# Performance work log

Measured on AMD Instinct MI355X. Metric: run time of the kernel, lower is better.

The kernel has to match this reference:

```python
import jax, jax.numpy as jnp
import numpy as np

B, S, D = 4, 4096, 1024
H, EXPAND, DCONV = 8, 2, 4
DI = D * EXPAND           # d_inner = 2048
HD = DI // H              # head_dim = 256
LN_EPS = 1e-5


def setup_inputs() -> dict:
    key = jax.random.key(0)
    ks = jax.random.split(key, 6)
    scale = lambda fan_in: 1.0 / np.sqrt(fan_in)
    return {
        "x": jax.random.normal(ks[0], (B, S, D), dtype=jnp.float32),
        "norm_w": jnp.ones((D,), dtype=jnp.float32),
        "norm_b": jnp.zeros((D,), dtype=jnp.float32),
        "in_proj_w": jax.random.normal(ks[1], (2 * DI, D), dtype=jnp.float32) * scale(D),
        "conv_w": jax.random.normal(ks[2], (DI, 1, DCONV), dtype=jnp.float32) * scale(DCONV),
        "conv_b": jax.random.normal(ks[3], (DI,), dtype=jnp.float32) * 0.02,
        "out_proj_w": jax.random.normal(ks[4], (D, DI), dtype=jnp.float32) * scale(DI),
        "log_alpha": jax.random.uniform(ks[5], (H,), dtype=jnp.float32,
                                        minval=np.log(0.1), maxval=np.log(0.99)),
    }


def reference(x, norm_w, norm_b, in_proj_w, conv_w, conv_b, out_proj_w, log_alpha):
    residual = x
    # LayerNorm
    mu = jnp.mean(x, axis=-1, keepdims=True)
    var = jnp.var(x, axis=-1, keepdims=True)
    xn = (x - mu) * jax.lax.rsqrt(var + LN_EPS) * norm_w + norm_b
    # input projection -> [B, S, 2*DI]
    xz = jnp.einsum("bsd,ed->bse", xn, in_proj_w)
    x_path, gate = xz[..., :DI], xz[..., DI:]
    # causal depthwise conv1d (torch pads d_conv-1 both sides then slices [:S])
    kernel = jnp.transpose(conv_w, (2, 1, 0))  # [DCONV, 1, DI] (WIO)
    x_path = jax.lax.conv_general_dilated(
        x_path, kernel, window_strides=(1,), padding=[(DCONV - 1, 0)],
        dimension_numbers=("NWC", "WIO", "NWC"), feature_group_count=DI,
    ) + conv_b
    # multi-head scalar-decay linear recurrence: y_t = alpha*y_{t-1} + x_t
    xh = x_path.reshape(B, S, H, HD)
    alpha = jax.nn.sigmoid(log_alpha)[:, None]  # [H, 1]

    def step(y, xt):
        y = alpha * y + xt
        return y, y

    y0 = jnp.zeros((B, H, HD), dtype=x.dtype)
    _, ys = jax.lax.scan(step, y0, jnp.transpose(xh, (1, 0, 2, 3)))  # [S, B, H, HD]
    x_path = jnp.transpose(ys, (1, 0, 2, 3)).reshape(B, S, DI)
    # gate + output projection (dropout in eval mode = identity)
    x_path = jax.nn.silu(x_path) * gate
    out = jnp.einsum("bse,de->bsd", x_path, out_proj_w)
    return out + residual
```

## Files before the change

### kernel.cpp

```cpp
#include <hip/hip_runtime.h>
#include <hip/hip_bf16.h>
#include <cstdint>

#define Bb 4
#define Ss 4096
#define Dd 1024
#define Hh 8
#define DI 2048
#define HD 256
#define XZN 4096
#define Mtot 16384
#define NCH 128
#define CHUNK 32

typedef __bf16 bf16_t;
typedef __bf16 bf16x8 __attribute__((ext_vector_type(8)));
typedef __bf16 bf16x4 __attribute__((ext_vector_type(4)));
typedef float f32x4 __attribute__((ext_vector_type(4)));

__device__ __forceinline__ float sigmoidf_(float x) { return 1.f / (1.f + __expf(-x)); }

__device__ __forceinline__ void async_ld16(void* lds, const void* g) {
  __builtin_amdgcn_global_load_lds(
      (const __attribute__((address_space(1))) void*)(uintptr_t)g,
      (__attribute__((address_space(3))) void*)(uint32_t)(uintptr_t)lds,
      16, 0, 0);
}

__global__ __launch_bounds__(256) void cvt_kernel(const float* __restrict__ s,
                                                  bf16_t* __restrict__ d) {
  const int i = blockIdx.x * 256 + threadIdx.x;
  const float4 v = ((const float4*)s)[i];
  bf16_t* o = d + 4 * (size_t)i;
  o[0] = (bf16_t)v.x; o[1] = (bf16_t)v.y; o[2] = (bf16_t)v.z; o[3] = (bf16_t)v.w;
}

__global__ __launch_bounds__(256) void ln_kernel(const float* __restrict__ x,
                                                 const float* __restrict__ w,
                                                 const float* __restrict__ b,
                                                 bf16_t* __restrict__ xn) {
  __shared__ float red[8];
  const int row = blockIdx.x;
  const float4 v = ((const float4*)(x + (size_t)row * Dd))[threadIdx.x];
  float s  = v.x + v.y + v.z + v.w;
  float s2 = v.x * v.x + v.y * v.y + v.z * v.z + v.w * v.w;
  #pragma unroll
  for (int off = 32; off; off >>= 1) { s += __shfl_down(s, off); s2 += __shfl_down(s2, off); }
  const int wave = threadIdx.x >> 6, lane = threadIdx.x & 63;
  if (lane == 0) { red[wave * 2] = s; red[wave * 2 + 1] = s2; }
  __syncthreads();
  if (threadIdx.x == 0) {
    float S = 0.f, S2 = 0.f;
    for (int i = 0; i < 4; ++i) { S += red[i * 2]; S2 += red[i * 2 + 1]; }
    red[0] = S; red[1] = S2;
  }
  __syncthreads();
  const float mean = red[0] * (1.f / Dd);
  const float var  = red[1] * (1.f / Dd) - mean * mean;
  const float rstd = rsqrtf(var + 1e-5f);
  const float4 wv = ((const float4*)w)[threadIdx.x];
  const float4 bv = ((const float4*)b)[threadIdx.x];
  bf16_t* o = xn + (size_t)row * Dd + threadIdx.x * 4;
  o[0] = (bf16_t)((v.x - mean) * rstd * wv.x + bv.x);
  o[1] = (bf16_t)((v.y - mean) * rstd * wv.y + bv.y);
  o[2] = (bf16_t)((v.z - mean) * rstd * wv.z + bv.z);
  o[3] = (bf16_t)((v.w - mean) * rstd * wv.w + bv.w);
}

template <int ADD_RES>
__global__ __launch_bounds__(512, 2) void gemm256(const bf16_t* __restrict__ A,
                                                  const bf16_t* __restrict__ Bw,
                                                  void* __restrict__ Cv,
                                                  const float* __restrict__ res,
                                                  int M, int N, int K) {
  __shared__ __align__(16) bf16_t As[4][8192];
  __shared__ __align__(16) bf16_t Bs[4][8192];
  const int tid = threadIdx.x;
  const int wave = tid >> 6, lane = tid & 63;
  const int wm = wave >> 2, wn = wave & 3;

  const int nbx = gridDim.x;
  const int nwg = nbx * gridDim.y;
  const int bid0 = blockIdx.y * nbx + blockIdx.x;
  const int cpx = nwg >> 3;
  const int bid = (bid0 & 7) * cpx + (bid0 >> 3);
  const int bm = bid / nbx, bn = bid % nbx;

  f32x4 acc[8][4];
  #pragma unroll
  for (int i = 0; i < 8; ++i)
    #pragma unroll
    for (int j = 0; j < 4; ++j) acc[i][j] = (f32x4){0.f, 0.f, 0.f, 0.f};

  const int srow = tid >> 2;
  const int sc   = (tid & 3) ^ ((tid >> 3) & 3);
  const bf16_t* Ag = A  + (size_t)(bm * 256 + srow) * K + sc * 8;
  const bf16_t* Bg = Bw + (size_t)(bn * 256 + srow) * K + sc * 8;
  const size_t rowK128 = (size_t)128 * K;
  char* const AsB = (char*)As + (wave << 10);
  char* const BsB = (char*)Bs + (wave << 10);

  const int fr = lane & 15, fq = lane >> 4;
  int aoff[8], boff[4];
  #pragma unroll
  for (int mt = 0; mt < 8; ++mt) {
    const int row = wm * 128 + mt * 16 + fr;
    aoff[mt] = row * 64 + ((fq ^ ((row >> 1) & 3)) << 4);
  }
  #pragma unroll
  for (int nt = 0; nt < 4; ++nt) {
    const int row = wn * 64 + nt * 16 + fr;
    boff[nt] = row * 64 + ((fq ^ ((row >> 1) & 3)) << 4);
  }

  const int NT = K >> 5;
  #pragma unroll
  for (int t = 0; t < 3; ++t) {
    const int kt = t << 5;
    async_ld16(AsB + t * 16384,        Ag + kt);
    async_ld16(AsB + t * 16384 + 8192, Ag + rowK128 + kt);
    async_ld16(BsB + t * 16384,        Bg + kt);
    async_ld16(BsB + t * 16384 + 8192, Bg + rowK128 + kt);
  }

  for (int t = 0; t < NT; ++t) {
    const int rem = NT - 1 - t;
    if (rem >= 2)      asm volatile("s_waitcnt vmcnt(8)" ::: "memory");
    else if (rem == 1) asm volatile("s_waitcnt vmcnt(4)" ::: "memory");
    else               asm volatile("s_waitcnt vmcnt(0)" ::: "memory");
    __builtin_amdgcn_s_barrier();

    const int buf = t & 3;
    const char* Ab = (const char*)As + buf * 16384;
    const char* Bbp = (const char*)Bs + buf * 16384;
    bf16x8 af[8], bfv[4];
    #pragma unroll
    for (int mt = 0; mt < 8; ++mt) af[mt] = *(const bf16x8*)(Ab + aoff[mt]);
    #pragma unroll
    for (int nt = 0; nt < 4; ++nt) bfv[nt] = *(const bf16x8*)(Bbp + boff[nt]);

    if (t + 3 < NT) {
      const int b = (t + 3) & 3;
      const int kt = (t + 3) << 5;
      async_ld16(AsB + b * 16384,        Ag + kt);
      async_ld16(AsB + b * 16384 + 8192, Ag + rowK128 + kt);
      async_ld16(BsB + b * 16384,        Bg + kt);
      async_ld16(BsB + b * 16384 + 8192, Bg + rowK128 + kt);
    }

    __builtin_amdgcn_s_setprio(1);
    #pragma unroll
    for (int mt = 0; mt < 8; ++mt)
      #pragma unroll
      for (int nt = 0; nt < 4; ++nt)
        acc[mt][nt] =
            __builtin_amdgcn_mfma_f32_16x16x32_bf16(af[mt], bfv[nt], acc[mt][nt], 0, 0, 0);
    __builtin_amdgcn_s_setprio(0);
  }

  const int m0 = bm * 256 + wm * 128 + fq * 4;
  const int n0 = bn * 256 + wn * 64 + fr;
  #pragma unroll
  for (int mt = 0; mt < 8; ++mt)
    #pragma unroll
    for (int nt = 0; nt < 4; ++nt)
      #pragma unroll
      for (int r = 0; r < 4; ++r) {
        const size_t m = (size_t)(m0 + mt * 16 + r);
        const size_t n = (size_t)(n0 + nt * 16);
        if (ADD_RES)
          ((float*)Cv)[m * N + n] = acc[mt][nt][r] + res[m * N + n];
        else
          ((bf16_t*)Cv)[m * N + n] = (bf16_t)acc[mt][nt][r];
      }
}

__global__ __launch_bounds__(256) void scanA_kernel(const bf16_t* __restrict__ xz,
                                                    const float* __restrict__ conv_w,
                                                    const float* __restrict__ conv_b,
                                                    const float* __restrict__ log_alpha,
                                                    float* __restrict__ carry) {
  const int half  = blockIdx.x & 1;
  const int chunk = (blockIdx.x >> 1) & (NCH - 1);
  const int b     = blockIdx.x >> 8;
  const int ch    = half * 1024 + threadIdx.x * 4;
  const float alpha = sigmoidf_(log_alpha[ch >> 8]);
  float w[4][4], bias[4];
  #pragma unroll
  for (int j = 0; j < 4; ++j) {
    const float4 cw = ((const float4*)conv_w)[ch + j];
    w[j][0] = cw.x; w[j][1] = cw.y; w[j][2] = cw.z; w[j][3] = cw.w;
    bias[j] = conv_b[ch + j];
  }
  const int s0 = chunk * CHUNK;
  const size_t base = ((size_t)b * Ss + s0) * XZN + ch;
  float x3[4] = {0,0,0,0}, x2[4] = {0,0,0,0}, x1[4] = {0,0,0,0}, y[4] = {0,0,0,0};
  if (chunk > 0) {
    const bf16x4 v3 = *(const bf16x4*)(xz + base - 3 * (size_t)XZN);
    const bf16x4 v2 = *(const bf16x4*)(xz + base - 2 * (size_t)XZN);
    const bf16x4 v1 = *(const bf16x4*)(xz + base - 1 * (size_t)XZN);
    #pragma unroll
    for (int j = 0; j < 4; ++j) { x3[j] = (float)v3[j]; x2[j] = (float)v2[j]; x1[j] = (float)v1[j]; }
  }
  #pragma unroll 4
  for (int t = 0; t < CHUNK; ++t) {
    const bf16x4 v = *(const bf16x4*)(xz + base + (size_t)t * XZN);
    #pragma unroll
    for (int j = 0; j < 4; ++j) {
      const float xc = (float)v[j];
      const float cv = bias[j] + w[j][0] * x3[j] + w[j][1] * x2[j] + w[j][2] * x1[j] + w[j][3] * xc;
      x3[j] = x2[j]; x2[j] = x1[j]; x1[j] = xc;
      y[j] = fmaf(alpha, y[j], cv);
    }
  }
  *(float4*)(carry + ((size_t)b * NCH + chunk) * DI + ch) =
      make_float4(y[0], y[1], y[2], y[3]);
}

__global__ __launch_bounds__(256) void scanB_kernel(const float* __restrict__ carry,
                                                    float* __restrict__ carryin,
                                                    const float* __restrict__ log_alpha) {
  __shared__ float S[8][32];
  const int b   = blockIdx.x >> 6;
  const int chg = blockIdx.x & 63;
  const int cg  = threadIdx.x >> 5;
  const int chl = threadIdx.x & 31;
  const int ch  = chg * 32 + chl;
  const float alpha = sigmoidf_(log_alpha[ch >> 8]);
  const float lal  = log2f(alpha);
  const float aL   = exp2f((float)CHUNK * lal);
  const float aL16 = exp2f((float)(CHUNK * 16) * lal);
  const size_t base = ((size_t)b * NCH + cg * 16) * DI + ch;
  float v[16];
  #pragma unroll
  for (int i = 0; i < 16; ++i) v[i] = carry[base + (size_t)i * DI];
  float Sl = v[0];
  #pragma unroll
  for (int i = 1; i < 16; ++i) Sl = fmaf(aL, Sl, v[i]);
  S[cg][chl] = Sl;
  __syncthreads();
  float P = 0.f;
  for (int h = 0; h < cg; ++h) P = fmaf(aL16, P, S[h][chl]);
  #pragma unroll
  for (int i = 0; i < 16; ++i) {
    carryin[base + (size_t)i * DI] = P;
    P = fmaf(aL, P, v[i]);
  }
}

__global__ __launch_bounds__(256) void scanC_kernel(const bf16_t* __restrict__ xz,
                                                    const float* __restrict__ conv_w,
                                                    const float* __restrict__ conv_b,
                                                    const float* __restrict__ log_alpha,
                                                    const float* __restrict__ carryin,
                                                    bf16_t* __restrict__ act) {
  const int half  = blockIdx.x & 1;
  const int chunk = (blockIdx.x >> 1) & (NCH - 1);
  const int b     = blockIdx.x >> 8;
  const int ch    = half * 1024 + threadIdx.x * 4;
  const float alpha = sigmoidf_(log_alpha[ch >> 8]);
  float w[4][4], bias[4];
  #pragma unroll
  for (int j = 0; j < 4; ++j) {
    const float4 cw = ((const float4*)conv_w)[ch + j];
    w[j][0] = cw.x; w[j][1] = cw.y; w[j][2] = cw.z; w[j][3] = cw.w;
    bias[j] = conv_b[ch + j];
  }
  const int s0 = chunk * CHUNK;
  const size_t base = ((size_t)b * Ss + s0) * XZN + ch;
  float x3[4] = {0,0,0,0}, x2[4] = {0,0,0,0}, x1[4] = {0,0,0,0}, y[4];
  const float4 cin = *(const float4*)(carryin + ((size_t)b * NCH + chunk) * DI + ch);
  y[0] = cin.x; y[1] = cin.y; y[2] = cin.z; y[3] = cin.w;
  if (chunk > 0) {
    const bf16x4 v3 = *(const bf16x4*)(xz + base - 3 * (size_t)XZN);
    const bf16x4 v2 = *(const bf16x4*)(xz + base - 2 * (size_t)XZN);
    const bf16x4 v1 = *(const bf16x4*)(xz + base - 1 * (size_t)XZN);
    #pragma unroll
    for (int j = 0; j < 4; ++j) { x3[j] = (float)v3[j]; x2[j] = (float)v2[j]; x1[j] = (float)v1[j]; }
  }
  const size_t abase = ((size_t)b * Ss + s0) * DI + ch;
  #pragma unroll 4
  for (int t = 0; t < CHUNK; ++t) {
    const bf16x4 v = *(const bf16x4*)(xz + base + (size_t)t * XZN);
    const bf16x4 gv = *(const bf16x4*)(xz + base + (size_t)t * XZN + DI);
    bf16x4 ov;
    #pragma unroll
    for (int j = 0; j < 4; ++j) {
      const float xc = (float)v[j];
      const float cv = bias[j] + w[j][0] * x3[j] + w[j][1] * x2[j] + w[j][2] * x1[j] + w[j][3] * xc;
      x3[j] = x2[j]; x2[j] = x1[j]; x1[j] = xc;
      y[j] = fmaf(alpha, y[j], cv);
      const float o = y[j] * (1.f / (1.f + __expf(-y[j]))) * (float)gv[j];
      ov[j] = (bf16_t)o;
    }
    *(bf16x4*)(act + abase + (size_t)t * DI) = ov;
  }
}

extern "C" void kernel_launch(void* const* d_in, const int* in_sizes, int n_in,
                              void* d_out, int out_size, void* d_ws, size_t ws_size,
                              hipStream_t stream) {
  const float* x          = (const float*)d_in[0];
  const float* norm_w     = (const float*)d_in[1];
  const float* norm_b     = (const float*)d_in[2];
  const float* in_proj_w  = (const float*)d_in[3];
  const float* conv_w     = (const float*)d_in[4];
  const float* conv_b     = (const float*)d_in[5];
  const float* out_proj_w = (const float*)d_in[6];
  const float* log_alpha  = (const float*)d_in[7];
  float* out = (float*)d_out;

  char* ws = (char*)d_ws;
  bf16_t* xn     = (bf16_t*)(ws);
  bf16_t* w_in   = (bf16_t*)(ws + 33554432);
  bf16_t* w_out  = (bf16_t*)(ws + 41943040);
  bf16_t* xz     = (bf16_t*)(ws + 46137344);
  bf16_t* act    = (bf16_t*)(ws + 180355072);
  float*  carry   = (float*)(ws);
  float*  carryin = (float*)(ws + 4194304);

  cvt_kernel<<<4096, 256, 0, stream>>>(in_proj_w, w_in);
  cvt_kernel<<<2048, 256, 0, stream>>>(out_proj_w, w_out);
  ln_kernel<<<Mtot, 256, 0, stream>>>(x, norm_w, norm_b, xn);

  dim3 g1(XZN / 256, Mtot / 256);
  gemm256<0><<<g1, 512, 0, stream>>>(xn, w_in, xz, nullptr, Mtot, XZN, Dd);

  scanA_kernel<<<Bb * NCH * 2, 256, 0, stream>>>(xz, conv_w, conv_b, log_alpha, carry);
  scanB_kernel<<<Bb * 64, 256, 0, stream>>>(carry, carryin, log_alpha);
  scanC_kernel<<<Bb * NCH * 2, 256, 0, stream>>>(xz, conv_w, conv_b, log_alpha, carryin, act);

  dim3 g2(Dd / 256, Mtot / 256);
  gemm256<1><<<g2, 512, 0, stream>>>(act, w_out, out, x, Mtot, Dd, DI);
}
```

Before: 407.8 us.

## Restructure GEMM main loop into double-buffered BK=64 ping-pong with interleaved staging

Replaces the 4-stage BK=32 ring of LDS buffers with two 64-wide K buffers. Each K-half's A fragments are split into two groups of four, and async global->LDS stores for the next tile are issued between fragment reads and MFMA groups. This lowers register pressure by holding fewer A fragments at once and spreads memory issue across the compute. In exchange the prefetch depth drops to one tile ahead and explicit lgkmcnt waits are added, which may expose more global latency; LDS use stays at 128KB per block.

```diff
diff --git a/kernel.cpp b/kernel.cpp
--- a/kernel.cpp
+++ b/kernel.cpp
@@ -73,8 +73,7 @@
                                                   void* __restrict__ Cv,
                                                   const float* __restrict__ res,
                                                   int M, int N, int K) {
-  __shared__ __align__(16) bf16_t As[4][8192];
-  __shared__ __align__(16) bf16_t Bs[4][8192];
+  __shared__ __align__(16) char LDS[131072];
   const int tid = threadIdx.x;
   const int wave = tid >> 6, lane = tid & 63;
   const int wm = wave >> 2, wn = wave & 3;
@@ -92,13 +91,11 @@
     #pragma unroll
     for (int j = 0; j < 4; ++j) acc[i][j] = (f32x4){0.f, 0.f, 0.f, 0.f};
 
-  const int srow = tid >> 2;
-  const int sc   = (tid & 3) ^ ((tid >> 3) & 3);
-  const bf16_t* Ag = A  + (size_t)(bm * 256 + srow) * K + sc * 8;
-  const bf16_t* Bg = Bw + (size_t)(bn * 256 + srow) * K + sc * 8;
+  const int scg = (lane & 3) ^ ((lane >> 3) & 3);
+  const bf16_t* Ag = A  + (size_t)(bm * 256 + wave * 16 + (lane >> 2)) * K + scg * 8;
+  const bf16_t* Bg = Bw + (size_t)(bn * 256 + wave * 16 + (lane >> 2)) * K + scg * 8;
   const size_t rowK128 = (size_t)128 * K;
-  char* const AsB = (char*)As + (wave << 10);
-  char* const BsB = (char*)Bs + (wave << 10);
+  char* const LDSw = LDS + wave * 1024;
 
   const int fr = lane & 15, fq = lane >> 4;
   int aoff[8], boff[4];
@@ -113,50 +110,87 @@
     boff[nt] = row * 64 + ((fq ^ ((row >> 1) & 3)) << 4);
   }
 
-  const int NT = K >> 5;
-  #pragma unroll
-  for (int t = 0; t < 3; ++t) {
-    const int kt = t << 5;
-    async_ld16(AsB + t * 16384,        Ag + kt);
-    async_ld16(AsB + t * 16384 + 8192, Ag + rowK128 + kt);
-    async_ld16(BsB + t * 16384,        Bg + kt);
-    async_ld16(BsB + t * 16384 + 8192, Bg + rowK128 + kt);
-  }
-
-  for (int t = 0; t < NT; ++t) {
-    const int rem = NT - 1 - t;
-    if (rem >= 2)      asm volatile("s_waitcnt vmcnt(8)" ::: "memory");
-    else if (rem == 1) asm volatile("s_waitcnt vmcnt(4)" ::: "memory");
-    else               asm volatile("s_waitcnt vmcnt(0)" ::: "memory");
-    __builtin_amdgcn_s_barrier();
-
-    const int buf = t & 3;
-    const char* Ab = (const char*)As + buf * 16384;
-    const char* Bbp = (const char*)Bs + buf * 16384;
-    bf16x8 af[8], bfv[4];
-    #pragma unroll
-    for (int mt = 0; mt < 8; ++mt) af[mt] = *(const bf16x8*)(Ab + aoff[mt]);
-    #pragma unroll
-    for (int nt = 0; nt < 4; ++nt) bfv[nt] = *(const bf16x8*)(Bbp + boff[nt]);
-
-    if (t + 3 < NT) {
-      const int b = (t + 3) & 3;
-      const int kt = (t + 3) << 5;
-      async_ld16(AsB + b * 16384,        Ag + kt);
-      async_ld16(AsB + b * 16384 + 8192, Ag + rowK128 + kt);
-      async_ld16(BsB + b * 16384,        Bg + kt);
-      async_ld16(BsB + b * 16384 + 8192, Bg + rowK128 + kt);
-    }
-
-    __builtin_amdgcn_s_setprio(1);
-    #pragma unroll
-    for (int mt = 0; mt < 8; ++mt)
-      #pragma unroll
-      for (int nt = 0; nt < 4; ++nt)
-        acc[mt][nt] =
-            __builtin_amdgcn_mfma_f32_16x16x32_bf16(af[mt], bfv[nt], acc[mt][nt], 0, 0, 0);
-    __builtin_amdgcn_s_setprio(0);
-  }
+  const int NT = K >> 6;
+
+#define STG(u, mat, ks) do {                                              \
+    char* d_ = LDSw + ((u) & 1) * 65536 + (mat) * 32768 + (ks) * 16384;   \
+    const bf16_t* s_ = (mat) ? Bg : Ag;                                   \
+    const int ko_ = (u) * 64 + (ks) * 32;                                 \
+    async_ld16(d_,        s_ + ko_);                                      \
+    async_ld16(d_ + 8192, s_ + rowK128 + ko_);                            \
+  } while (0)
+
+#define RDA(DST, bufb, ks, g) do {                                        \
+    _Pragma("unroll")                                                     \
+    for (int i_ = 0; i_ < 4; ++i_)                                        \
+      DST[i_] = *(const bf16x8*)(LDS + (bufb) * 65536 + (ks) * 16384 + aoff[(g) * 4 + i_]); \
+  } while (0)
+
+#define RDB(DST, bufb, ks) do {                                           \
+    _Pragma("unroll")                                                     \
+    for (int i_ = 0; i_ < 4; ++i_)                                        \
+      DST[i_] = *(const bf16x8*)(LDS + (bufb) * 65536 + 32768 + (ks) * 16384 + boff[i_]); \
+  } while (0)
+
+#define MM(AF, BF, g) do {                                                \
+    __builtin_amdgcn_s_setprio(1);                                        \
+    _Pragma("unroll")                                                     \
+    for (int m_ = 0; m_ < 4; ++m_)                                        \
+      _Pragma("unroll")                                                   \
+      for (int n_ = 0; n_ < 4; ++n_)                                      \
+        acc[(g) * 4 + m_][n_] = __builtin_amdgcn_mfma_f32_16x16x32_bf16(  \
+            AF[m_], BF[n_], acc[(g) * 4 + m_][n_], 0, 0, 0);              \
+    __builtin_amdgcn_s_setprio(0);                                        \
+  } while (0)
+
+#define LGKM0 do { asm volatile("s_waitcnt lgkmcnt(0)" ::: "memory");     \
+    __builtin_amdgcn_sched_barrier(0); } while (0)
+#define VMB4 do { asm volatile("s_waitcnt vmcnt(4)" ::: "memory");        \
+    __builtin_amdgcn_s_barrier(); } while (0)
+#define VMB0 do { asm volatile("s_waitcnt vmcnt(0)" ::: "memory");        \
+    __builtin_amdgcn_s_barrier(); } while (0)
+
+  STG(0, 0, 0); STG(0, 1, 0); STG(0, 0, 1); STG(0, 1, 1);
+  bf16x8 af[4], ag[4], bfk[4];
+
+  for (int t = 0; t < NT - 1; ++t) {
+    const int cb = t & 1;
+    VMB4;
+    RDB(bfk, cb, 0); RDA(af, cb, 0, 0);
+    STG(t + 1, 0, 0);
+    LGKM0; MM(af, bfk, 0);
+    RDA(ag, cb, 0, 1);
+    STG(t + 1, 1, 0);
+    LGKM0; MM(ag, bfk, 1);
+    VMB4;
+    RDB(bfk, cb, 1); RDA(af, cb, 1, 0);
+    STG(t + 1, 0, 1);
+    LGKM0; MM(af, bfk, 0);
+    RDA(ag, cb, 1, 1);
+    STG(t + 1, 1, 1);
+    LGKM0; MM(ag, bfk, 1);
+  }
+  {
+    const int cb = (NT - 1) & 1;
+    VMB4;
+    RDB(bfk, cb, 0); RDA(af, cb, 0, 0);
+    LGKM0; MM(af, bfk, 0);
+    RDA(ag, cb, 0, 1);
+    LGKM0; MM(ag, bfk, 1);
+    VMB0;
+    RDB(bfk, cb, 1); RDA(af, cb, 1, 0);
+    LGKM0; MM(af, bfk, 0);
+    RDA(ag, cb, 1, 1);
+    LGKM0; MM(ag, bfk, 1);
+  }
+
+#undef STG
+#undef RDA
+#undef RDB
+#undef MM
+#undef LGKM0
+#undef VMB4
+#undef VMB0
 
   const int m0 = bm * 256 + wm * 128 + fq * 4;
   const int n0 = bn * 256 + wn * 64 + fr;
```

Measured after the change: 392.2 us. 1.04x faster.
